# Optimization experiments

Hardware: AMD Instinct MI355X
Metric: run time of the kernel (lower is better)

The kernel has to match this reference:

```python
import jax, jax.numpy as jnp
import numpy as np

K_GF = 8      # neighbors used by graph filtering
EPS = 1e-5    # BatchNorm eps
B, CW, SD, M = 32, 512, 16, 2048


def _conv1x1(x, w, b):
    # x: [B, Cin, M], w: [Cout, Cin], b: [Cout]
    return jnp.einsum('oi,bim->bom', w, x) + b[None, :, None]


def _bn(x, g, be):
    # training-mode BatchNorm1d over (batch, points)
    mu = jnp.mean(x, axis=(0, 2), keepdims=True)
    var = jnp.var(x, axis=(0, 2), keepdims=True)
    return g[None, :, None] * (x - mu) * jax.lax.rsqrt(var + EPS) + be[None, :, None]


def _graph_filtering(x):
    # x: [B, 3, M]  -> sharpening filter over kNN graph: out = 2*x - mean(neighbors)
    pts = jnp.transpose(x, (0, 2, 1))                      # [B, M, 3]
    sq = jnp.sum(pts * pts, axis=-1)                       # [B, M]
    d = sq[:, :, None] + sq[:, None, :] - 2.0 * jnp.einsum('bmc,bnc->bmn', pts, pts)
    idx = jax.lax.top_k(-d, K_GF + 1)[1][..., 1:]          # [B, M, K] drop self
    neigh = jax.vmap(lambda p, i: p[i])(pts, idx)          # [B, M, K, 3]
    out = 2.0 * pts - jnp.mean(neigh, axis=2)
    return jnp.transpose(out, (0, 2, 1))


def setup_inputs() -> dict:
    key = jax.random.key(0)
    ks = jax.random.split(key, 12)
    def w(k, o, i):
        return jax.random.normal(k, (o, i), jnp.float32) * (1.0 / np.sqrt(i))
    h = [256, CW, 512, 256, 128, 64]
    inp = {
        'z': jax.random.normal(ks[0], (B, CW), jnp.float32),
        's': jax.random.normal(ks[1], (B, SD, M), jnp.float32),
        'w_m1': w(ks[2], h[0], SD), 'b_m1': jnp.zeros((h[0],), jnp.float32),
        'w_m2': w(ks[3], h[1], h[0]), 'b_m2': jnp.zeros((h[1],), jnp.float32),
        'w_out': w(ks[4], 3, h[5]), 'b_out': jnp.zeros((3,), jnp.float32),
    }
    for j, (ci, co) in enumerate(zip(h[1:-1], h[2:])):
        inp[f'w_c{j}'] = w(ks[5 + j], co, ci)
        inp[f'b_c{j}'] = jnp.zeros((co,), jnp.float32)
        inp[f'g_c{j}'] = jnp.ones((co,), jnp.float32)
        inp[f'be_c{j}'] = jnp.zeros((co,), jnp.float32)
    return inp


def reference(z, s, w_m1, b_m1, w_m2, b_m2, w_out, b_out,
              w_c0, b_c0, g_c0, be_c0, w_c1, b_c1, g_c1, be_c1,
              w_c2, b_c2, g_c2, be_c2, w_c3, b_c3, g_c3, be_c3):
    x = s / jnp.linalg.norm(s, axis=1, keepdims=True)          # unit samples
    x = jax.nn.relu(_conv1x1(x, w_m1, b_m1))                   # map_samples1
    x = jnp.clip(_conv1x1(x, w_m2, b_m2), -1.0, 1.0)           # map_samples2 (Hardtanh)
    x = z[:, :, None] * x                                      # z-modulation
    for w_, b_, g_, be_ in ((w_c0, b_c0, g_c0, be_c0), (w_c1, b_c1, g_c1, be_c1),
                            (w_c2, b_c2, g_c2, be_c2), (w_c3, b_c3, g_c3, be_c3)):
        x = jax.nn.relu(_bn(_conv1x1(x, w_, b_), g_, be_))
    x = _conv1x1(x, w_out, b_out)                              # [B, 3, M]
    return _graph_filtering(x)
```

## Files before the change

kernel.cpp:

```cpp
#include <hip/hip_runtime.h>
#include <math.h>

#define Bn 32
#define Mn 2048
#define Nn 65536
#define Hn 32768
#define SDn 16
#define CWn 512
#define EPSf 1e-5f
#define KGF 8
#define WTOT 573440
#define LSC 2048.0f
#define LSCI (1.0f / 2048.0f)

typedef unsigned short u16;
typedef _Float16 fp16_t;
typedef __attribute__((ext_vector_type(8))) _Float16 h8v;
typedef __attribute__((ext_vector_type(4))) float f4v;

__device__ __forceinline__ u16 f2h(float f) {
    union { fp16_t h; u16 u; } c; c.h = (fp16_t)f; return c.u;
}
__device__ __forceinline__ float h2f(u16 u) {
    union { fp16_t h; u16 u; } c; c.u = u; return (float)c.h;
}
__device__ __forceinline__ void fsplit(float f, u16& hi, u16& lo) {
    hi = f2h(f);
    lo = f2h((f - h2f(hi)) * LSC);
}
__device__ __forceinline__ float fjoin(u16 hi, u16 lo) {
    return h2f(hi) + h2f(lo) * LSCI;
}
__device__ __forceinline__ void gll16(const u16* g, u16* l) {
    __builtin_amdgcn_global_load_lds((const __attribute__((address_space(1))) void*)g,
                                     (__attribute__((address_space(3))) void*)l, 16, 0, 0);
}
__device__ __forceinline__ unsigned umin(unsigned a, unsigned b) { return a < b ? a : b; }
__device__ __forceinline__ unsigned umax(unsigned a, unsigned b) { return a > b ? a : b; }

__global__ __launch_bounds__(256) void prep_kernel(
    const float* __restrict__ wm1, const float* __restrict__ wm2,
    const float* __restrict__ wc0, const float* __restrict__ wc1,
    const float* __restrict__ wc2, const float* __restrict__ wc3,
    const float* __restrict__ s,
    u16* __restrict__ wbuf, u16* __restrict__ xs, float* __restrict__ stats)
{
    const int bid = blockIdx.x;
    const int tid = threadIdx.x;
    if (bid < 2240) {
        int i = bid * 256 + tid;
        float w; int r, k, Cin; size_t base;
        if (i < 8192) {
            r = i >> 5; k = i & 31; Cin = 32; base = 0;
            w = (k < SDn) ? wm1[r * SDn + k] : 0.f;
        } else {
            int j = i - 8192;
            if (j < 131072)                    { r = j >> 8; k = j & 255; Cin = 256; base = 16384;   w = wm2[j]; }
            else if ((j -= 131072) < 262144)   { r = j >> 9; k = j & 511; Cin = 512; base = 278528;  w = wc0[j]; }
            else if ((j -= 262144) < 131072)   { r = j >> 9; k = j & 511; Cin = 512; base = 802816;  w = wc1[j]; }
            else if ((j -= 131072) < 32768)    { r = j >> 8; k = j & 255; Cin = 256; base = 1064960; w = wc2[j]; }
            else { j -= 32768;                   r = j >> 7; k = j & 127; Cin = 128; base = 1130496; w = wc3[j]; }
        }
        const size_t addr = base + (size_t)r * (2 * Cin) + k;
        u16 hi, lo; fsplit(w, hi, lo);
        wbuf[addr] = hi;
        wbuf[addr + Cin] = lo;
    } else if (bid < 2496) {
        const int b2 = bid - 2240;
        const int m = (b2 & 7) * 256 + tid;
        const int b = b2 >> 3;
        const float* sp = s + (size_t)b * SDn * Mn + m;
        float v[SDn]; float sq = 0.f;
#pragma unroll
        for (int c = 0; c < SDn; ++c) { v[c] = sp[(size_t)c * Mn]; sq += v[c] * v[c]; }
        const float r = 1.0f / sqrtf(sq);
        unsigned int uh[8], ul[8];
#pragma unroll
        for (int c = 0; c < 8; ++c) {
            u16 h0, l0, h1, l1;
            fsplit(v[2 * c] * r, h0, l0);
            fsplit(v[2 * c + 1] * r, h1, l1);
            uh[c] = (unsigned int)h0 | ((unsigned int)h1 << 16);
            ul[c] = (unsigned int)l0 | ((unsigned int)l1 << 16);
        }
        uint4* xp = (uint4*)(xs + (size_t)(b * Mn + m) * 64);
        xp[0] = make_uint4(uh[0], uh[1], uh[2], uh[3]);
        xp[1] = make_uint4(uh[4], uh[5], uh[6], uh[7]);
        xp[2] = make_uint4(0, 0, 0, 0);
        xp[3] = make_uint4(0, 0, 0, 0);
        xp[4] = make_uint4(ul[0], ul[1], ul[2], ul[3]);
        xp[5] = make_uint4(ul[4], ul[5], ul[6], ul[7]);
        xp[6] = make_uint4(0, 0, 0, 0);
        xp[7] = make_uint4(0, 0, 0, 0);
    } else {
        float4 z4 = {0.f, 0.f, 0.f, 0.f};
        float4* sp4 = (float4*)stats;
#pragma unroll
        for (int k = 0; k < 4; ++k) sp4[tid * 4 + k] = z4;
    }
}

template<int RW, int CWv, int EPI, int MY, int IBN, int CINT, int NT>
__global__ __launch_bounds__(NT) void mfma_gemm(
    const u16* __restrict__ W, const u16* __restrict__ X, u16* __restrict__ Y,
    const float* __restrict__ bias, const float* __restrict__ zmod,
    const float* __restrict__ statsIn, const float* __restrict__ gin,
    const float* __restrict__ bein, float* __restrict__ stats, int Cout)
{
    constexpr int BM = RW * 64, BN = CWv * 64;
    constexpr int ASEG = (BM * 4) / NT;
    constexpr int BSEG = (BN * 4) / NT;
    constexpr int LMY = (MY == 1) ? 0 : (MY == 2) ? 1 : (MY == 4) ? 2 : 3;
    constexpr int SW = 2 * CINT;
    constexpr int NST = CINT >> 5;
    constexpr int VMSTEP = 2 * ASEG + 2 * BSEG;
    constexpr int SSTATN = (EPI == 2) ? (CWv * BM * 2) : 1;
    constexpr int BNN = IBN ? (CINT * 2) : 1;
    constexpr int AUXN = (SSTATN > BNN) ? SSTATN : BNN;
    __shared__ __align__(16) u16 Ah[2][BM * 32], Al[2][BM * 32];
    __shared__ __align__(16) u16 Bh[2][BN * 32], Bl[2][BN * 32];
    __shared__ float saux[AUXN];

    const int tid = threadIdx.x;
    const int wave = tid >> 6;
    const int lane = tid & 63;
    const int wm = wave & (RW - 1), wn = wave / RW;
    const int l15 = lane & 15, q = lane >> 4;
    const int lin = blockIdx.x;
    const int xcd = lin & 7;
    const int jj = lin >> 3;
    const int m0 = (jj & (MY - 1)) * BM;
    const int n0 = (xcd + ((jj >> LMY) << 3)) * BN;

    f4v acc0[4][4], accL[4][4];
#pragma unroll
    for (int i = 0; i < 4; ++i)
#pragma unroll
        for (int j = 0; j < 4; ++j) {
            acc0[i][j] = (f4v){0.f, 0.f, 0.f, 0.f};
            accL[i][j] = (f4v){0.f, 0.f, 0.f, 0.f};
        }

    auto stageAB = [&](int ks, int buf) {
        const int k0 = ks << 5;
#pragma unroll
        for (int s = 0; s < ASEG; ++s) {
            const int flat = s * NT + tid;
            const int row = flat >> 2;
            const int qs = (flat & 3) ^ ((row >> 1) & 3);
            const u16* ga = W + (size_t)(m0 + row) * SW + k0 + qs * 8;
            gll16(ga, Ah[buf] + flat * 8);
            gll16(ga + CINT, Al[buf] + flat * 8);
        }
#pragma unroll
        for (int s = 0; s < BSEG; ++s) {
            const int flat = s * NT + tid;
            const int row = flat >> 2;
            const int qs = (flat & 3) ^ ((row >> 1) & 3);
            const u16* gb = X + (size_t)(n0 + row) * SW + k0 + qs * 8;
            gll16(gb, Bh[buf] + flat * 8);
            gll16(gb + CINT, Bl[buf] + flat * 8);
        }
    };

    if constexpr (IBN) {
        const float inv = 1.0f / (float)Nn;
        for (int c = tid; c < CINT; c += NT) {
            const float mean = statsIn[c * 2] * inv;
            const float var = statsIn[c * 2 + 1] * inv - mean * mean;
            const float sc = gin[c] / sqrtf(var + EPSf);
            saux[c * 2] = sc;
            saux[c * 2 + 1] = fmaf(-mean, sc, bein[c]);
        }
        asm volatile("s_waitcnt vmcnt(0) lgkmcnt(0)" ::: "memory");
    }
    stageAB(0, 0);
    if constexpr (NST > 1) stageAB(1, 1);

#pragma unroll 1
    for (int ks = 0; ks < NST; ++ks) {
        const int cur = ks & 1;
        if (ks + 1 < NST) {
            asm volatile("s_waitcnt vmcnt(%0)" :: "n"(VMSTEP) : "memory");
        } else {
            asm volatile("s_waitcnt vmcnt(0)" ::: "memory");
        }
        __builtin_amdgcn_s_barrier();
        __builtin_amdgcn_sched_barrier(0);
        h8v afh[4], afl[4], bfh[4], bfl[4];
#pragma unroll
        for (int i = 0; i < 4; ++i) {
            const int ar = wm * 64 + i * 16 + l15;
            const int ao = ar * 32 + ((q ^ ((ar >> 1) & 3)) << 3);
            afh[i] = *(const h8v*)(Ah[cur] + ao);
            afl[i] = *(const h8v*)(Al[cur] + ao);
        }
#pragma unroll
        for (int j = 0; j < 4; ++j) {
            const int br = wn * 64 + j * 16 + l15;
            const int bo = br * 32 + ((q ^ ((br >> 1) & 3)) << 3);
            bfh[j] = *(const h8v*)(Bh[cur] + bo);
            bfl[j] = *(const h8v*)(Bl[cur] + bo);
        }
        if constexpr (IBN) {
            const int kb = ((ks << 5) + q * 8) * 2;
            const float4 p0 = *(const float4*)(saux + kb);
            const float4 p1 = *(const float4*)(saux + kb + 4);
            const float4 p2 = *(const float4*)(saux + kb + 8);
            const float4 p3 = *(const float4*)(saux + kb + 12);
            const float sc8[8] = {p0.x, p0.z, p1.x, p1.z, p2.x, p2.z, p3.x, p3.z};
            const float sh8[8] = {p0.y, p0.w, p1.y, p1.w, p2.y, p2.w, p3.y, p3.w};
#pragma unroll
            for (int j = 0; j < 4; ++j) {
#pragma unroll
                for (int e = 0; e < 8; ++e) {
                    const float v = (float)bfh[j][e] + (float)bfl[j][e] * LSCI;
                    const float a = fmaxf(fmaf(v, sc8[e], sh8[e]), 0.f);
                    const fp16_t hh = (fp16_t)a;
                    bfh[j][e] = hh;
                    bfl[j][e] = (fp16_t)((a - (float)hh) * LSC);
                }
            }
        }
        __builtin_amdgcn_s_setprio(1);
#pragma unroll
        for (int i = 0; i < 4; ++i)
#pragma unroll
            for (int j = 0; j < 4; ++j)
                accL[i][j] = __builtin_amdgcn_mfma_f32_16x16x32_f16(afh[i], bfl[j], accL[i][j], 0, 0, 0);
#pragma unroll
        for (int i = 0; i < 4; ++i)
#pragma unroll
            for (int j = 0; j < 4; ++j)
                acc0[i][j] = __builtin_amdgcn_mfma_f32_16x16x32_f16(afh[i], bfh[j], acc0[i][j], 0, 0, 0);
#pragma unroll
        for (int i = 0; i < 4; ++i)
#pragma unroll
            for (int j = 0; j < 4; ++j)
                accL[i][j] = __builtin_amdgcn_mfma_f32_16x16x32_f16(afl[i], bfh[j], accL[i][j], 0, 0, 0);
        __builtin_amdgcn_s_setprio(0);
        __builtin_amdgcn_s_barrier();
        if (ks + 2 < NST) stageAB(ks + 2, cur);
    }

    float* sstat = saux;
    const int bb = n0 >> 11;
    const int SY = 2 * Cout;
#pragma unroll
    for (int i = 0; i < 4; ++i) {
        const int chb = m0 + wm * 64 + i * 16 + q * 4;
        const float4 bias4 = *(const float4*)(bias + chb);
        float z0 = 0.f, z1 = 0.f, z2 = 0.f, z3 = 0.f;
        if constexpr (EPI == 1) {
            const float4 z4 = *(const float4*)(zmod + bb * CWn + chb);
            z0 = z4.x; z1 = z4.y; z2 = z4.z; z3 = z4.w;
        }
        float ssum[4] = {0.f, 0.f, 0.f, 0.f}, ssq[4] = {0.f, 0.f, 0.f, 0.f};
#pragma unroll
        for (int j = 0; j < 4; ++j) {
            const int n = n0 + wn * 64 + j * 16 + l15;
            float v0 = fmaf(accL[i][j][0], LSCI, acc0[i][j][0]) + bias4.x;
            float v1 = fmaf(accL[i][j][1], LSCI, acc0[i][j][1]) + bias4.y;
            float v2 = fmaf(accL[i][j][2], LSCI, acc0[i][j][2]) + bias4.z;
            float v3 = fmaf(accL[i][j][3], LSCI, acc0[i][j][3]) + bias4.w;
            if constexpr (EPI == 0) {
                v0 = fmaxf(v0, 0.f); v1 = fmaxf(v1, 0.f); v2 = fmaxf(v2, 0.f); v3 = fmaxf(v3, 0.f);
            } else if constexpr (EPI == 1) {
                v0 = fminf(fmaxf(v0, -1.f), 1.f) * z0;
                v1 = fminf(fmaxf(v1, -1.f), 1.f) * z1;
                v2 = fminf(fmaxf(v2, -1.f), 1.f) * z2;
                v3 = fminf(fmaxf(v3, -1.f), 1.f) * z3;
            } else {
                ssum[0] += v0; ssum[1] += v1; ssum[2] += v2; ssum[3] += v3;
                ssq[0] += v0 * v0; ssq[1] += v1 * v1; ssq[2] += v2 * v2; ssq[3] += v3 * v3;
            }
            u16 h0, l0, h1, l1, h2, l2, h3, l3;
            fsplit(v0, h0, l0); fsplit(v1, h1, l1);
            fsplit(v2, h2, l2); fsplit(v3, h3, l3);
            ushort4 hv = {h0, h1, h2, h3};
            ushort4 lv = {l0, l1, l2, l3};
            u16* yp = Y + (size_t)n * SY + chb;
            *(ushort4*)yp = hv;
            *(ushort4*)(yp + Cout) = lv;
        }
        if constexpr (EPI == 2) {
#pragma unroll
            for (int r = 0; r < 4; ++r) {
#pragma unroll
                for (int d = 1; d < 16; d <<= 1) {
                    ssum[r] += __shfl_xor(ssum[r], d);
                    ssq[r]  += __shfl_xor(ssq[r], d);
                }
            }
            if (l15 == 0) {
                const int chl = wm * 64 + i * 16 + q * 4;
#pragma unroll
                for (int r = 0; r < 4; ++r) {
                    sstat[(wn * BM + chl + r) * 2]     = ssum[r];
                    sstat[(wn * BM + chl + r) * 2 + 1] = ssq[r];
                }
            }
        }
    }
    if constexpr (EPI == 2) {
        __syncthreads();
        if (tid < BM) {
            float s0 = 0.f, s1 = 0.f;
#pragma unroll
            for (int w = 0; w < CWv; ++w) {
                s0 += sstat[(w * BM + tid) * 2];
                s1 += sstat[(w * BM + tid) * 2 + 1];
            }
            atomicAdd(&stats[(m0 + tid) * 2], s0);
            atomicAdd(&stats[(m0 + tid) * 2 + 1], s1);
        }
    }
}

__global__ __launch_bounds__(256) void finalconv_pm(
    const u16* __restrict__ y3, const float* __restrict__ statsIn,
    const float* __restrict__ gin, const float* __restrict__ bein,
    const float* __restrict__ wout, const float* __restrict__ bout,
    float* __restrict__ pts)
{
    __shared__ float swo[3][64];
    __shared__ float ssc[64], ssh[64];
    const int tid = threadIdx.x;
    if (tid < 192) swo[tid / 64][tid % 64] = wout[tid];
    if (tid < 64) {
        const float inv = 1.0f / (float)Nn;
        const float mean = statsIn[tid * 2] * inv;
        const float var = statsIn[tid * 2 + 1] * inv - mean * mean;
        const float sc = gin[tid] / sqrtf(var + EPSf);
        ssc[tid] = sc;
        ssh[tid] = fmaf(-mean, sc, bein[tid]);
    }
    __syncthreads();
    const int n = blockIdx.x * 256 + tid;
    const uint4* yph = (const uint4*)(y3 + (size_t)n * 128);
    float d0 = bout[0], d1 = bout[1], d2 = bout[2];
#pragma unroll
    for (int cc = 0; cc < 8; ++cc) {
        const uint4 H = yph[cc];
        const uint4 L = yph[8 + cc];
        const unsigned hu[4] = {H.x, H.y, H.z, H.w};
        const unsigned lu[4] = {L.x, L.y, L.z, L.w};
#pragma unroll
        for (int e = 0; e < 4; ++e) {
            const int c = cc * 8 + e * 2;
            const float v0 = fjoin((u16)(hu[e] & 0xffff), (u16)(lu[e] & 0xffff));
            const float v1 = fjoin((u16)(hu[e] >> 16), (u16)(lu[e] >> 16));
            const float a0 = fmaxf(fmaf(v0, ssc[c], ssh[c]), 0.f);
            const float a1 = fmaxf(fmaf(v1, ssc[c + 1], ssh[c + 1]), 0.f);
            d0 = fmaf(a0, swo[0][c], d0); d0 = fmaf(a1, swo[0][c + 1], d0);
            d1 = fmaf(a0, swo[1][c], d1); d1 = fmaf(a1, swo[1][c + 1], d1);
            d2 = fmaf(a0, swo[2][c], d2); d2 = fmaf(a1, swo[2][c + 1], d2);
        }
    }
    float4 p = {d0, d1, d2, d0 * d0 + d1 * d1 + d2 * d2};
    *(float4*)(pts + (size_t)n * 4) = p;
}

__global__ __launch_bounds__(512) void knn_kernel(const float* __restrict__ pts,
                                                  float* __restrict__ out) {
    __shared__ __align__(16) float4 sp[Mn];
    const int b = blockIdx.y;
    const int tid = threadIdx.x;
    const float4* pb = (const float4*)pts + (size_t)b * Mn;
    for (int i = tid; i < Mn; i += 512) sp[i] = pb[i];
    __syncthreads();
    const int lane = tid & 63;
    const int wv = tid >> 6;
    const int seg = lane & 15;
    const int ptl = (wv << 2) | (lane >> 4);
    const int m = blockIdx.x * 32 + ptl;
    const float4 p = sp[m];
    const int cself = (seg == (m >> 7)) ? (m & 127) : 128;
    const int nb = seg << 7;
    unsigned bk[8];
#pragma unroll
    for (int k = 0; k < 8; ++k) bk[k] = 0xFFFFFFFFu;
    for (int t = 0; t < 128; ++t) {
        const int tt = (t + seg) & 127;
        const float4 q = sp[nb | tt];
        const float dot = fmaf(p.x, q.x, fmaf(p.y, q.y, p.z * q.z));
        float d = fmaf(-2.f, dot, q.w + p.w);
        d = fmaxf(d, 0.f);
        unsigned key = (__float_as_uint(d) & 0xFFFFFF80u) | (unsigned)tt;
        key = (tt == cself) ? 0xFFFFFFFFu : key;
        bk[7] = umin(bk[7], key);
#pragma unroll
        for (int k = 6; k >= 0; --k) {
            const unsigned lo = umin(bk[k], bk[k + 1]);
            bk[k + 1] = umax(bk[k], bk[k + 1]);
            bk[k] = lo;
        }
    }
    unsigned ok[8];
#pragma unroll
    for (int k = 0; k < 8; ++k) ok[k] = bk[k];
#pragma unroll
    for (int r = 1; r <= 8; r <<= 1) {
        unsigned od[8], md[8];
#pragma unroll
        for (int k = 0; k < 8; ++k) od[k] = (unsigned)__shfl_xor((int)bk[k], r);
#pragma unroll
        for (int k = 0; k < 8; ++k) md[k] = umin(bk[k], od[7 - k]);
#define CSU(a, c) { const unsigned lo_ = umin(md[a], md[c]); md[c] = umax(md[a], md[c]); md[a] = lo_; }
        CSU(0,4); CSU(1,5); CSU(2,6); CSU(3,7);
        CSU(0,2); CSU(1,3); CSU(4,6); CSU(5,7);
        CSU(0,1); CSU(2,3); CSU(4,5); CSU(6,7);
#undef CSU
#pragma unroll
        for (int k = 0; k < 8; ++k) bk[k] = md[k];
    }
    const unsigned TK = bk[7];
    float slt[4] = {0.f, 0.f, 0.f, 0.f};
    float seq[4] = {0.f, 0.f, 0.f, 0.f};
#pragma unroll
    for (int k = 0; k < 8; ++k) {
        const unsigned key = ok[k];
        const float4 q = sp[nb | (int)(key & 127u)];
        const bool lt = key < TK;
        const bool eq = key == TK;
        slt[0] += lt ? q.x : 0.f; slt[1] += lt ? q.y : 0.f;
        slt[2] += lt ? q.z : 0.f; slt[3] += lt ? 1.f : 0.f;
        seq[0] += eq ? q.x : 0.f; seq[1] += eq ? q.y : 0.f;
        seq[2] += eq ? q.z : 0.f; seq[3] += eq ? 1.f : 0.f;
    }
#pragma unroll
    for (int r = 1; r <= 8; r <<= 1) {
#pragma unroll
        for (int k = 0; k < 4; ++k) {
            slt[k] += __shfl_xor(slt[k], r);
            seq[k] += __shfl_xor(seq[k], r);
        }
    }
    if (seg == 0) {
        const float scale = (8.f - slt[3]) / seq[3];
        const float nx = fmaf(scale, seq[0], slt[0]);
        const float ny = fmaf(scale, seq[1], slt[1]);
        const float nz = fmaf(scale, seq[2], slt[2]);
        const float s8 = 0.125f;
        float* ob = out + (size_t)b * 3 * Mn;
        ob[m]          = 2.f * p.x - nx * s8;
        ob[Mn + m]     = 2.f * p.y - ny * s8;
        ob[2 * Mn + m] = 2.f * p.z - nz * s8;
    }
}

extern "C" void kernel_launch(void* const* d_in, const int* in_sizes, int n_in,
                              void* d_out, int out_size, void* d_ws, size_t ws_size,
                              hipStream_t stream)
{
    (void)in_sizes; (void)n_in; (void)out_size;
    const float* z     = (const float*)d_in[0];
    const float* s     = (const float*)d_in[1];
    const float* w_m1  = (const float*)d_in[2];
    const float* b_m1  = (const float*)d_in[3];
    const float* w_m2  = (const float*)d_in[4];
    const float* b_m2  = (const float*)d_in[5];
    const float* w_out = (const float*)d_in[6];
    const float* b_out = (const float*)d_in[7];
    const float* w_c[4]  = {(const float*)d_in[8],  (const float*)d_in[12], (const float*)d_in[16], (const float*)d_in[20]};
    const float* b_c[4]  = {(const float*)d_in[9],  (const float*)d_in[13], (const float*)d_in[17], (const float*)d_in[21]};
    const float* g_c[4]  = {(const float*)d_in[10], (const float*)d_in[14], (const float*)d_in[18], (const float*)d_in[22]};
    const float* be_c[4] = {(const float*)d_in[11], (const float*)d_in[15], (const float*)d_in[19], (const float*)d_in[23]};

    char* ws = (char*)d_ws;
    const size_t MB = 1024ull * 1024ull;
    float* outp = (float*)d_out;
    if (ws_size < 208 * MB) return;

    u16*   wbuf  = (u16*)ws;
    float* stats = (float*)(ws + 3 * MB);
    u16*   xs  = (u16*)(ws + 4 * MB);
    u16*   x1  = (u16*)(ws + 12 * MB);
    u16*   x2  = (u16*)(ws + 76 * MB);
    u16*   y0  = (u16*)(ws + 12 * MB);
    u16*   y0a = (u16*)(ws + 12 * MB);
    u16*   y0b = (u16*)(ws + 76 * MB);
    u16*   y1  = (u16*)(ws + 140 * MB);
    u16*   y2  = (u16*)(ws + 12 * MB);
    u16*   y3  = (u16*)(ws + 76 * MB);
    float* pts = (float*)(ws + 4 * MB);

    prep_kernel<<<2497, 256, 0, stream>>>(w_m1, w_m2, w_c[0], w_c[1], w_c[2], w_c[3], s, wbuf, xs, stats);
    mfma_gemm<2, 2, 0, 2, 0, 32, 256><<<1024, 256, 0, stream>>>(wbuf, xs, x1, b_m1, nullptr, nullptr, nullptr, nullptr, nullptr, 256);
    mfma_gemm<4, 2, 1, 2, 0, 256, 512><<<1024, 512, 0, stream>>>(wbuf + 16384, x1, x2, b_m2, z, nullptr, nullptr, nullptr, nullptr, 512);
    mfma_gemm<4, 2, 2, 2, 0, 512, 512><<<512, 512, 0, stream>>>(wbuf + 278528, x2, y0a, b_c[0], nullptr, nullptr, nullptr, nullptr, stats + 0, 512);
    mfma_gemm<4, 2, 2, 2, 0, 512, 512><<<512, 512, 0, stream>>>(wbuf + 278528, x2 + (size_t)Hn * 1024, y0b, b_c[0], nullptr, nullptr, nullptr, nullptr, stats + 0, 512);
    mfma_gemm<4, 2, 2, 1, 1, 512, 512><<<512, 512, 0, stream>>>(wbuf + 802816, y0, y1, b_c[1], nullptr, stats + 0, g_c[0], be_c[0], stats + 1024, 256);
    mfma_gemm<2, 2, 2, 1, 1, 256, 256><<<512, 256, 0, stream>>>(wbuf + 1064960, y1, y2, b_c[2], nullptr, stats + 1024, g_c[1], be_c[1], stats + 2048, 128);
    mfma_gemm<1, 4, 2, 1, 1, 128, 256><<<256, 256, 0, stream>>>(wbuf + 1130496, y2, y3, b_c[3], nullptr, stats + 2048, g_c[2], be_c[2], stats + 3072, 64);
    finalconv_pm<<<Nn / 256, 256, 0, stream>>>(y3, stats + 3072, g_c[3], be_c[3], w_out, b_out, pts);
    knn_kernel<<<dim3(Mn / 32, Bn), 512, 0, stream>>>(pts, outp);
}
```

Before: 603.4 us.

## Stage GEMM epilogue through LDS bounce buffer for coalesced 16-byte stores

The GEMM epilogue now writes each 16-column slab of fp16 hi/lo outputs into a padded shared-memory bounce buffer. It then copies the slab to global memory as contiguous 16-byte vectors, replacing the scattered 8-byte per-lane stores. BN statistics are kept per row-group until the end. The layer-c2 GEMM launch also moves to a wider tile (4 column waves, 512 threads, half the blocks). The cost is extra LDS, more barriers in the epilogue, and possibly lower occupancy.

Measured after the change: 537.9 us. 10.9% less time.

```diff
diff --git a/kernel.cpp b/kernel.cpp
--- a/kernel.cpp
+++ b/kernel.cpp
@@ -107,6 +107,7 @@
     const float* __restrict__ statsIn, const float* __restrict__ gin,
     const float* __restrict__ bein, float* __restrict__ stats, int Cout)
 {
+    static_assert(NT == RW * CWv * 64, "wave grid must exactly cover the tile");
     constexpr int BM = RW * 64, BN = CWv * 64;
     constexpr int ASEG = (BM * 4) / NT;
     constexpr int BSEG = (BN * 4) / NT;
@@ -117,8 +118,13 @@
     constexpr int SSTATN = (EPI == 2) ? (CWv * BM * 2) : 1;
     constexpr int BNN = IBN ? (CINT * 2) : 1;
     constexpr int AUXN = (SSTATN > BNN) ? SSTATN : BNN;
+    constexpr int BSTR = 2 * BM + 8;
+    constexpr int BROWS = CWv * 16;
+    constexpr int UNITS = BROWS * 2 * (BM / 8);
+    static_assert(UNITS % NT == 0, "store units must tile the block");
     __shared__ __align__(16) u16 Ah[2][BM * 32], Al[2][BM * 32];
     __shared__ __align__(16) u16 Bh[2][BN * 32], Bl[2][BN * 32];
+    __shared__ __align__(16) u16 bounce[BROWS * BSTR];
     __shared__ float saux[AUXN];
 
     const int tid = threadIdx.x;
@@ -246,19 +252,21 @@
     float* sstat = saux;
     const int bb = n0 >> 11;
     const int SY = 2 * Cout;
-#pragma unroll
-    for (int i = 0; i < 4; ++i) {
-        const int chb = m0 + wm * 64 + i * 16 + q * 4;
-        const float4 bias4 = *(const float4*)(bias + chb);
-        float z0 = 0.f, z1 = 0.f, z2 = 0.f, z3 = 0.f;
-        if constexpr (EPI == 1) {
-            const float4 z4 = *(const float4*)(zmod + bb * CWn + chb);
-            z0 = z4.x; z1 = z4.y; z2 = z4.z; z3 = z4.w;
-        }
-        float ssum[4] = {0.f, 0.f, 0.f, 0.f}, ssq[4] = {0.f, 0.f, 0.f, 0.f};
-#pragma unroll
-        for (int j = 0; j < 4; ++j) {
-            const int n = n0 + wn * 64 + j * 16 + l15;
+    float ssum[4][4], ssq[4][4];
+    if constexpr (EPI == 2) {
+#pragma unroll
+        for (int i = 0; i < 4; ++i)
+#pragma unroll
+            for (int r = 0; r < 4; ++r) { ssum[i][r] = 0.f; ssq[i][r] = 0.f; }
+    }
+    const int nl_w = wn * 16 + l15;
+#pragma unroll
+    for (int j = 0; j < 4; ++j) {
+        __builtin_amdgcn_s_barrier();
+#pragma unroll
+        for (int i = 0; i < 4; ++i) {
+            const int chb = m0 + wm * 64 + i * 16 + q * 4;
+            const float4 bias4 = *(const float4*)(bias + chb);
             float v0 = fmaf(accL[i][j][0], LSCI, acc0[i][j][0]) + bias4.x;
             float v1 = fmaf(accL[i][j][1], LSCI, acc0[i][j][1]) + bias4.y;
             float v2 = fmaf(accL[i][j][2], LSCI, acc0[i][j][2]) + bias4.z;
@@ -266,43 +274,57 @@
             if constexpr (EPI == 0) {
                 v0 = fmaxf(v0, 0.f); v1 = fmaxf(v1, 0.f); v2 = fmaxf(v2, 0.f); v3 = fmaxf(v3, 0.f);
             } else if constexpr (EPI == 1) {
-                v0 = fminf(fmaxf(v0, -1.f), 1.f) * z0;
-                v1 = fminf(fmaxf(v1, -1.f), 1.f) * z1;
-                v2 = fminf(fmaxf(v2, -1.f), 1.f) * z2;
-                v3 = fminf(fmaxf(v3, -1.f), 1.f) * z3;
+                const float4 z4 = *(const float4*)(zmod + bb * CWn + chb);
+                v0 = fminf(fmaxf(v0, -1.f), 1.f) * z4.x;
+                v1 = fminf(fmaxf(v1, -1.f), 1.f) * z4.y;
+                v2 = fminf(fmaxf(v2, -1.f), 1.f) * z4.z;
+                v3 = fminf(fmaxf(v3, -1.f), 1.f) * z4.w;
             } else {
-                ssum[0] += v0; ssum[1] += v1; ssum[2] += v2; ssum[3] += v3;
-                ssq[0] += v0 * v0; ssq[1] += v1 * v1; ssq[2] += v2 * v2; ssq[3] += v3 * v3;
+                ssum[i][0] += v0; ssum[i][1] += v1; ssum[i][2] += v2; ssum[i][3] += v3;
+                ssq[i][0] += v0 * v0; ssq[i][1] += v1 * v1; ssq[i][2] += v2 * v2; ssq[i][3] += v3 * v3;
             }
             u16 h0, l0, h1, l1, h2, l2, h3, l3;
             fsplit(v0, h0, l0); fsplit(v1, h1, l1);
             fsplit(v2, h2, l2); fsplit(v3, h3, l3);
-            ushort4 hv = {h0, h1, h2, h3};
-            ushort4 lv = {l0, l1, l2, l3};
-            u16* yp = Y + (size_t)n * SY + chb;
-            *(ushort4*)yp = hv;
-            *(ushort4*)(yp + Cout) = lv;
-        }
-        if constexpr (EPI == 2) {
+            const ushort4 hv = {h0, h1, h2, h3};
+            const ushort4 lv = {l0, l1, l2, l3};
+            const int chl = wm * 64 + i * 16 + q * 4;
+            *(ushort4*)(bounce + nl_w * BSTR + chl) = hv;
+            *(ushort4*)(bounce + nl_w * BSTR + BM + chl) = lv;
+        }
+        __builtin_amdgcn_s_barrier();
+#pragma unroll
+        for (int u0 = 0; u0 < UNITS; u0 += NT) {
+            const int u = u0 + tid;
+            const int nl = u / (2 * (BM / 8));
+            const int rem = u % (2 * (BM / 8));
+            const int plane = rem / (BM / 8);
+            const int off8 = rem % (BM / 8);
+            const int n = n0 + (nl >> 4) * 64 + j * 16 + (nl & 15);
+            u16* yp = Y + (size_t)n * SY + (plane ? Cout : 0) + m0 + off8 * 8;
+            *(uint4*)yp = *(const uint4*)(bounce + nl * BSTR + plane * BM + off8 * 8);
+        }
+    }
+    if constexpr (EPI == 2) {
+#pragma unroll
+        for (int i = 0; i < 4; ++i) {
 #pragma unroll
             for (int r = 0; r < 4; ++r) {
 #pragma unroll
                 for (int d = 1; d < 16; d <<= 1) {
-                    ssum[r] += __shfl_xor(ssum[r], d);
-                    ssq[r]  += __shfl_xor(ssq[r], d);
+                    ssum[i][r] += __shfl_xor(ssum[i][r], d);
+                    ssq[i][r]  += __shfl_xor(ssq[i][r], d);
                 }
             }
             if (l15 == 0) {
                 const int chl = wm * 64 + i * 16 + q * 4;
 #pragma unroll
                 for (int r = 0; r < 4; ++r) {
-                    sstat[(wn * BM + chl + r) * 2]     = ssum[r];
-                    sstat[(wn * BM + chl + r) * 2 + 1] = ssq[r];
+                    sstat[(wn * BM + chl + r) * 2]     = ssum[i][r];
+                    sstat[(wn * BM + chl + r) * 2 + 1] = ssq[i][r];
                 }
             }
         }
-    }
-    if constexpr (EPI == 2) {
         __syncthreads();
         if (tid < BM) {
             float s0 = 0.f, s1 = 0.f;
@@ -491,7 +513,7 @@
     mfma_gemm<4, 2, 2, 2, 0, 512, 512><<<512, 512, 0, stream>>>(wbuf + 278528, x2, y0a, b_c[0], nullptr, nullptr, nullptr, nullptr, stats + 0, 512);
     mfma_gemm<4, 2, 2, 2, 0, 512, 512><<<512, 512, 0, stream>>>(wbuf + 278528, x2 + (size_t)Hn * 1024, y0b, b_c[0], nullptr, nullptr, nullptr, nullptr, stats + 0, 512);
     mfma_gemm<4, 2, 2, 1, 1, 512, 512><<<512, 512, 0, stream>>>(wbuf + 802816, y0, y1, b_c[1], nullptr, stats + 0, g_c[0], be_c[0], stats + 1024, 256);
-    mfma_gemm<2, 2, 2, 1, 1, 256, 256><<<512, 256, 0, stream>>>(wbuf + 1064960, y1, y2, b_c[2], nullptr, stats + 1024, g_c[1], be_c[1], stats + 2048, 128);
+    mfma_gemm<2, 4, 2, 1, 1, 256, 512><<<256, 512, 0, stream>>>(wbuf + 1064960, y1, y2, b_c[2], nullptr, stats + 1024, g_c[1], be_c[1], stats + 2048, 128);
     mfma_gemm<1, 4, 2, 1, 1, 128, 256><<<256, 256, 0, stream>>>(wbuf + 1130496, y2, y3, b_c[3], nullptr, stats + 2048, g_c[2], be_c[2], stats + 3072, 64);
     finalconv_pm<<<Nn / 256, 256, 0, stream>>>(y3, stats + 3072, g_c[3], be_c[3], w_out, b_out, pts);
     knn_kernel<<<dim3(Mn / 32, Bn), 512, 0, stream>>>(pts, outp);
```
